# Performance work log

Measured on AMD Instinct MI355X. Metric: run time of the kernel, lower is better.

The kernel has to match this reference:

```python
import jax, jax.numpy as jnp
import numpy as np

NUM_EXPERTS = 8
HIDDEN = 2048
FFN = 1376
CAPACITY_FACTOR = 1.25
SCORE_SCALE = 1.0


def setup_inputs() -> dict:
    key = jax.random.key(0)
    k = jax.random.split(key, 6)
    T = 8192
    x = jax.random.normal(k[0], (T, HIDDEN), dtype=jnp.float32)
    topK_indices = jax.random.randint(k[1], (T,), 0, NUM_EXPERTS, dtype=jnp.int64)
    topK_scores = jax.random.uniform(k[2], (T,), dtype=jnp.float32)
    s = 1.0 / np.sqrt(HIDDEN)
    w_gate = jax.random.normal(k[3], (NUM_EXPERTS, HIDDEN, FFN), dtype=jnp.float32) * s
    w_up = jax.random.normal(k[4], (NUM_EXPERTS, HIDDEN, FFN), dtype=jnp.float32) * s
    w_down = jax.random.normal(k[5], (NUM_EXPERTS, FFN, HIDDEN), dtype=jnp.float32) * (1.0 / np.sqrt(FFN))
    return {"x": x, "topK_indices": topK_indices, "topK_scores": topK_scores,
            "w_gate": w_gate, "w_up": w_up, "w_down": w_down}


def reference(x, topK_indices, topK_scores, w_gate, w_up, w_down):
    T, D = x.shape
    E = w_gate.shape[0]
    capacity = int(CAPACITY_FACTOR * T / E)  # static (depends only on shapes)
    # position of each token within its assigned expert (deterministic drop:
    # keep the first `capacity` tokens in sequence order per expert)
    oh = jax.nn.one_hot(topK_indices, E, dtype=jnp.int32)          # [T,E]
    rank = jnp.take_along_axis(jnp.cumsum(oh, axis=0) - 1,
                               topK_indices[:, None].astype(jnp.int32), axis=1)[:, 0]
    keep = rank < capacity                                          # [T]
    # dispatch into per-expert capacity buffers; dropped tokens go to dummy slot
    slot = jnp.where(keep, topK_indices.astype(jnp.int32) * capacity + rank, E * capacity)
    buf = jnp.zeros((E * capacity + 1, D), x.dtype)
    buf = buf.at[slot].set(jnp.where(keep[:, None], x, jnp.zeros_like(x)))
    xe = buf[:E * capacity].reshape(E, capacity, D)                 # [E,C,D]
    # per-expert SwiGLU MLP as grouped GEMMs
    h = jax.nn.silu(jnp.einsum('ecd,edf->ecf', xe, w_gate)) * jnp.einsum('ecd,edf->ecf', xe, w_up)
    out = jnp.einsum('ecf,efd->ecd', h, w_down).reshape(E * capacity, D)
    out = jnp.concatenate([out, jnp.zeros((1, D), out.dtype)], axis=0)
    # combine: dropped tokens -> zero (dropped_padding='zero'), gate-score fusion
    y = out[slot] * keep[:, None].astype(out.dtype)
    y = y * (topK_scores[:, None] * SCORE_SCALE)
    return y
```

## Files before the change

kernel.cpp:

```cpp
#include <hip/hip_runtime.h>
#include <hip/hip_bf16.h>
#include <cstdint>
#include <cstddef>

#define NTOK 8192
#define DH   2048
#define DF   1376
#define DFP  1408
#define NE   8
#define CAP  1280

typedef __bf16 bf16x8 __attribute__((ext_vector_type(8)));
typedef float  f32x4  __attribute__((ext_vector_type(4)));

#define BARRIER() asm volatile("s_barrier" ::: "memory")
#define WAITV0()  asm volatile("s_waitcnt vmcnt(0)" ::: "memory")
#define WAITV4()  asm volatile("s_waitcnt vmcnt(4)" ::: "memory")
#define WAITV6()  asm volatile("s_waitcnt vmcnt(6)" ::: "memory")
#define SETPRIO(n) __builtin_amdgcn_s_setprio(n)

__device__ __forceinline__ uint32_t pk2(float a, float b) {
  float2 f; f.x = a; f.y = b;
  union { __hip_bfloat162 h; uint32_t u; } cv;
  cv.h = __float22bfloat162_rn(f);
  return cv.u;
}
__device__ __forceinline__ ushort bf16bits(float a) {
  return (ushort)(pk2(a, 0.f) & 0xFFFFu);
}
__device__ __forceinline__ void gload16(const ushort* g, ushort* l) {
  __builtin_amdgcn_global_load_lds(
      (const __attribute__((address_space(1))) uint32_t*)(const void*)g,
      (__attribute__((address_space(3))) uint32_t*)(void*)l,
      16, 0, 0);
}

__global__ void routing_kernel(const int* __restrict__ idx, int* __restrict__ tok_slot,
                               int* __restrict__ tok_keep) {
  __shared__ int cnt[256][NE];
  const int t = threadIdx.x;
  for (int s = t; s < NE * CAP; s += 256) tok_slot[s] = -1;
  unsigned long long cA = 0ull, cB = 0ull;
  const int per = NTOK / 256, base = t * per;
  for (int i = 0; i < per; ++i) {
    int e = idx[base + i];
    unsigned long long inc = 1ull << ((e & 3) * 16);
    if (e < 4) cA += inc; else cB += inc;
  }
#pragma unroll
  for (int e = 0; e < 4; ++e) cnt[t][e]     = (int)((cA >> (e * 16)) & 0xFFFF);
#pragma unroll
  for (int e = 0; e < 4; ++e) cnt[t][4 + e] = (int)((cB >> (e * 16)) & 0xFFFF);
  __syncthreads();
  if (t < NE) {
    int run = 0;
    for (int i = 0; i < 256; ++i) { int c = cnt[i][t]; cnt[i][t] = run; run += c; }
  }
  __syncthreads();
  cA = 0ull; cB = 0ull;
#pragma unroll
  for (int e = 0; e < 4; ++e) cA |= (unsigned long long)(cnt[t][e] & 0xFFFF) << (e * 16);
#pragma unroll
  for (int e = 0; e < 4; ++e) cB |= (unsigned long long)(cnt[t][4 + e] & 0xFFFF) << (e * 16);
  for (int i = 0; i < per; ++i) {
    int token = base + i;
    int e = idx[token];
    int sh = (e & 3) * 16;
    int r = (int)(((e < 4 ? cA : cB) >> sh) & 0xFFFF);
    unsigned long long inc = 1ull << sh;
    if (e < 4) cA += inc; else cB += inc;
    bool keep = (r < CAP);
    tok_keep[token] = keep ? 1 : 0;
    if (keep) tok_slot[e * CAP + r] = token;
  }
}

__global__ void zero_dropped(const int* __restrict__ keep, float* __restrict__ y) {
  if (keep[blockIdx.x]) return;
  float4 z = {0.f, 0.f, 0.f, 0.f};
  float* p = y + (size_t)blockIdx.x * DH + threadIdx.x * 8;
  *(float4*)p = z;
  *(float4*)(p + 4) = z;
}

__global__ void convert_x(const float* __restrict__ x, ushort* __restrict__ xb) {
  int i = (blockIdx.x * 256 + threadIdx.x) * 8;
  float4 a = *(const float4*)(x + i);
  float4 b = *(const float4*)(x + i + 4);
  uint4 p = { pk2(a.x, a.y), pk2(a.z, a.w), pk2(b.x, b.y), pk2(b.z, b.w) };
  *(uint4*)(xb + i) = p;
}

__global__ __launch_bounds__(256) void transpose_cvt(
    const float* __restrict__ in, ushort* __restrict__ out, int K, int N) {
  __shared__ ushort T[64][72];
  const int tid = threadIdx.x;
  const int n0 = blockIdx.x * 64, k0 = blockIdx.y * 64;
  const size_t eoff_in  = (size_t)blockIdx.z * K * N;
  const size_t eoff_out = (size_t)blockIdx.z * N * K;
  const int kr = tid >> 4;
  const int nc = (tid & 15) * 4;
#pragma unroll
  for (int it = 0; it < 4; ++it) {
    int k = k0 + kr + it * 16;
    int n = n0 + nc;
    float4 v = {0.f, 0.f, 0.f, 0.f};
    if (k < K && n + 4 <= N) v = *(const float4*)(in + eoff_in + (size_t)k * N + n);
    T[nc + 0][kr + it * 16] = bf16bits(v.x);
    T[nc + 1][kr + it * 16] = bf16bits(v.y);
    T[nc + 2][kr + it * 16] = bf16bits(v.z);
    T[nc + 3][kr + it * 16] = bf16bits(v.w);
  }
  __syncthreads();
  const int nr = tid >> 2;
  const int kc = tid & 3;
#pragma unroll
  for (int it = 0; it < 2; ++it) {
    int kloc = kc * 16 + it * 8;
    int n = n0 + nr, k = k0 + kloc;
    if (n < N && k + 8 <= K)
      *(uint4*)(out + eoff_out + (size_t)n * K + k) = *(const uint4*)&T[nr][kloc];
  }
}

__global__ void pad_h(ushort* __restrict__ h) {
  int idx = blockIdx.x * 512 + threadIdx.x;
  int row = idx >> 2, q = idx & 3;
  uint4 z = {0u, 0u, 0u, 0u};
  *(uint4*)(h + (size_t)row * DFP + DF + q * 8) = z;
}

__global__ __launch_bounds__(512, 1) void gemm_gateup3(
    const ushort* __restrict__ xb, const ushort* __restrict__ wgt,
    const ushort* __restrict__ wut, const int* __restrict__ tok_slot,
    ushort* __restrict__ h)
{
  __shared__ __align__(16) char smbuf[131072];
  char* sm = smbuf;
  const int tid = threadIdx.x, lane = tid & 63, wid = tid >> 6;
  const int wr = wid >> 1, wc = wid & 1;
  const int l15 = lane & 15, l4 = lane >> 4;

  int wgid = (blockIdx.x & 7) * 55 + (blockIdx.x >> 3);
  const int e = wgid / 55;
  const int rem = wgid - e * 55;
  const int mt = rem / 11, nt = rem - (rem / 11) * 11;
  const int n0 = nt * 128;

  const ushort* srcA[2][2]; const ushort* srcBg[2]; const ushort* srcBu[2];
#pragma unroll
  for (int u = 0; u < 2; ++u)
#pragma unroll
    for (int jj = 0; jj < 2; ++jj) {
      int o = u * 16384 + (jj * 8 + wid) * 1024 + lane * 16;
      int os = o ^ (((o >> 7) & 7) << 4);
      int row = os >> 7, kb = os & 127;
      int tk = tok_slot[e * CAP + mt * 256 + row];
      if (tk < 0) tk = 0;
      srcA[u][jj] = xb + (size_t)tk * DH + (kb >> 1);
    }
#pragma unroll
  for (int jj = 0; jj < 2; ++jj) {
    int o = (jj * 8 + wid) * 1024 + lane * 16;
    int os = o ^ (((o >> 7) & 7) << 4);
    int row = os >> 7, kb = os & 127;
    int n = n0 + row; if (n > DF - 1) n = DF - 1;
    srcBg[jj] = wgt + ((size_t)e * DF + n) * DH + (kb >> 1);
    srcBu[jj] = wut + ((size_t)e * DF + n) * DH + (kb >> 1);
  }
  int aoff0[4], aoff1[4], boff0[4], boff1[4];
#pragma unroll
  for (int i = 0; i < 4; ++i) {
    int row = wr * 64 + i * 16 + l15;
    int r4 = (row & 7) << 4;
    aoff0[i] = row * 128 + ((l4 * 16) ^ r4);
    aoff1[i] = row * 128 + ((l4 * 16 + 64) ^ r4);
  }
#pragma unroll
  for (int j = 0; j < 4; ++j) {
    int row = wc * 64 + j * 16 + l15;
    int r4 = (row & 7) << 4;
    boff0[j] = row * 128 + ((l4 * 16) ^ r4);
    boff1[j] = row * 128 + ((l4 * 16 + 64) ^ r4);
  }
  const int dst0 = wid * 1024, dst1 = (8 + wid) * 1024;

  f32x4 accG[4][4], accU[4][4];
#pragma unroll
  for (int i = 0; i < 4; ++i)
#pragma unroll
    for (int j = 0; j < 4; ++j) {
      accG[i][j] = (f32x4){0.f, 0.f, 0.f, 0.f};
      accU[i][j] = (f32x4){0.f, 0.f, 0.f, 0.f};
    }

  const int NT = DH / 64;
  gload16(srcA[0][0], (ushort*)(sm + dst0));
  gload16(srcA[0][1], (ushort*)(sm + dst1));
  gload16(srcA[1][0], (ushort*)(sm + 16384 + dst0));
  gload16(srcA[1][1], (ushort*)(sm + 16384 + dst1));
  gload16(srcBg[0],   (ushort*)(sm + 65536 + dst0));
  gload16(srcBg[1],   (ushort*)(sm + 65536 + dst1));
  gload16(srcBu[0],   (ushort*)(sm + 98304 + dst0));
  gload16(srcBu[1],   (ushort*)(sm + 98304 + dst1));
  gload16(srcA[0][0] + 64, (ushort*)(sm + 32768 + dst0));
  gload16(srcA[0][1] + 64, (ushort*)(sm + 32768 + dst1));
  gload16(srcA[1][0] + 64, (ushort*)(sm + 32768 + 16384 + dst0));
  gload16(srcA[1][1] + 64, (ushort*)(sm + 32768 + 16384 + dst1));
  gload16(srcBg[0] + 64,   (ushort*)(sm + 65536 + 16384 + dst0));
  gload16(srcBg[1] + 64,   (ushort*)(sm + 65536 + 16384 + dst1));
  WAITV6();
  BARRIER();

  bf16x8 a0[4], a1[4], bg[4], bu[4];
  for (int t = 0; t < NT; ++t) {
    const int p = t & 1;
    char* Ab  = sm + p * 32768;
    char* Bgb = sm + 65536 + p * 16384;
    char* Bub = sm + 98304 + p * 16384;
    char* Bun = sm + 98304 + (p ^ 1) * 16384;
#pragma unroll
    for (int i = 0; i < 4; ++i) a0[i] = *(const bf16x8*)(Ab + aoff0[i]);
#pragma unroll
    for (int j = 0; j < 4; ++j) bg[j] = *(const bf16x8*)(Bgb + boff0[j]);
    if (t + 1 < NT) {
      int kk = (t + 1) * 64;
      gload16(srcBu[0] + kk, (ushort*)(Bun + dst0));
      gload16(srcBu[1] + kk, (ushort*)(Bun + dst1));
    }
    BARRIER();
    SETPRIO(1);
#pragma unroll
    for (int j = 0; j < 4; ++j)
#pragma unroll
      for (int i = 0; i < 4; ++i)
        accG[i][j] = __builtin_amdgcn_mfma_f32_16x16x32_bf16(a0[i], bg[j], accG[i][j], 0, 0, 0);
    SETPRIO(0);
    BARRIER();
#pragma unroll
    for (int i = 0; i < 4; ++i) a1[i] = *(const bf16x8*)(Ab + aoff1[i]);
#pragma unroll
    for (int j = 0; j < 4; ++j) bg[j] = *(const bf16x8*)(Bgb + boff1[j]);
    BARRIER();
    SETPRIO(1);
#pragma unroll
    for (int j = 0; j < 4; ++j)
#pragma unroll
      for (int i = 0; i < 4; ++i)
        accG[i][j] = __builtin_amdgcn_mfma_f32_16x16x32_bf16(a1[i], bg[j], accG[i][j], 0, 0, 0);
    SETPRIO(0);
    BARRIER();
#pragma unroll
    for (int j = 0; j < 4; ++j) bu[j] = *(const bf16x8*)(Bub + boff0[j]);
    if (t + 2 < NT) {
      int kk = (t + 2) * 64;
      gload16(srcA[0][0] + kk, (ushort*)(Ab + dst0));
      gload16(srcA[0][1] + kk, (ushort*)(Ab + dst1));
      gload16(srcBg[0] + kk,   (ushort*)(Bgb + dst0));
      gload16(srcBg[1] + kk,   (ushort*)(Bgb + dst1));
    }
    BARRIER();
    SETPRIO(1);
#pragma unroll
    for (int j = 0; j < 4; ++j)
#pragma unroll
      for (int i = 0; i < 4; ++i)
        accU[i][j] = __builtin_amdgcn_mfma_f32_16x16x32_bf16(a0[i], bu[j], accU[i][j], 0, 0, 0);
    SETPRIO(0);
    BARRIER();
#pragma unroll
    for (int j = 0; j < 4; ++j) bu[j] = *(const bf16x8*)(Bub + boff1[j]);
    if (t + 2 < NT) {
      int kk = (t + 2) * 64;
      gload16(srcA[1][0] + kk, (ushort*)(Ab + 16384 + dst0));
      gload16(srcA[1][1] + kk, (ushort*)(Ab + 16384 + dst1));
    }
    BARRIER();
    SETPRIO(1);
#pragma unroll
    for (int j = 0; j < 4; ++j)
#pragma unroll
      for (int i = 0; i < 4; ++i)
        accU[i][j] = __builtin_amdgcn_mfma_f32_16x16x32_bf16(a1[i], bu[j], accU[i][j], 0, 0, 0);
    SETPRIO(0);
    if (t >= NT - 2) { WAITV0(); } else { WAITV6(); }
    BARRIER();
  }
  const size_t rowbase = (size_t)(e * CAP + mt * 256 + wr * 64);
#pragma unroll
  for (int j = 0; j < 4; ++j) {
    int col = n0 + wc * 64 + j * 16 + l15;
    if (col < DF) {
#pragma unroll
      for (int i = 0; i < 4; ++i)
#pragma unroll
        for (int r = 0; r < 4; ++r) {
          size_t row = rowbase + i * 16 + l4 * 4 + r;
          float gv = accG[i][j][r], uv = accU[i][j][r];
          h[row * DFP + col] = bf16bits(gv / (1.f + __expf(-gv)) * uv);
        }
    }
  }
}

__global__ __launch_bounds__(512, 1) void gemm_down3(
    const ushort* __restrict__ h, const ushort* __restrict__ wdt,
    const int* __restrict__ tok_slot, const float* __restrict__ scores,
    float* __restrict__ y)
{
  __shared__ __align__(16) char smbuf[100352];
  char* sm = smbuf;
  int* tokc = (int*)(sm + 98304);
  float* scc = (float*)(sm + 99328);
  const int tid = threadIdx.x, lane = tid & 63, wid = tid >> 6;
  const int wr = wid >> 1, wc = wid & 1;
  const int l15 = lane & 15, l4 = lane >> 4;

  int wgid = (blockIdx.x & 7) * 80 + (blockIdx.x >> 3);
  const int e = wgid / 80;
  const int rem = wgid - e * 80;
  const int mt = rem / 16, nt = rem & 15;
  const int n0 = nt * 128;

  if (tid < 256) {
    int tk = tok_slot[e * CAP + mt * 256 + tid];
    tokc[tid] = tk;
    scc[tid] = (tk >= 0) ? scores[tk] : 0.f;
  }
  __syncthreads();

  const size_t hrow0 = (size_t)(e * CAP + mt * 256);
  const ushort* srcA[2][2]; const ushort* srcB[2];
#pragma unroll
  for (int u = 0; u < 2; ++u)
#pragma unroll
    for (int jj = 0; jj < 2; ++jj) {
      int o = u * 16384 + (jj * 8 + wid) * 1024 + lane * 16;
      int os = o ^ (((o >> 7) & 7) << 4);
      int row = os >> 7, kb = os & 127;
      srcA[u][jj] = h + (hrow0 + row) * DFP + (kb >> 1);
    }
#pragma unroll
  for (int jj = 0; jj < 2; ++jj) {
    int o = (jj * 8 + wid) * 1024 + lane * 16;
    int os = o ^ (((o >> 7) & 7) << 4);
    int row = os >> 7, kb = os & 127;
    srcB[jj] = wdt + ((size_t)e * DH + n0 + row) * DF + (kb >> 1);
  }
  int aoff0[4], aoff1[4], boff0[4], boff1[4];
#pragma unroll
  for (int i = 0; i < 4; ++i) {
    int row = wr * 64 + i * 16 + l15;
    int r4 = (row & 7) << 4;
    aoff0[i] = row * 128 + ((l4 * 16) ^ r4);
    aoff1[i] = row * 128 + ((l4 * 16 + 64) ^ r4);
  }
#pragma unroll
  for (int j = 0; j < 4; ++j) {
    int row = wc * 64 + j * 16 + l15;
    int r4 = (row & 7) << 4;
    boff0[j] = row * 128 + ((l4 * 16) ^ r4);
    boff1[j] = row * 128 + ((l4 * 16 + 64) ^ r4);
  }
  const int dst0 = wid * 1024, dst1 = (8 + wid) * 1024;

  f32x4 acc[4][4];
#pragma unroll
  for (int i = 0; i < 4; ++i)
#pragma unroll
    for (int j = 0; j < 4; ++j) acc[i][j] = (f32x4){0.f, 0.f, 0.f, 0.f};

  const int NT = DFP / 64;
  gload16(srcA[0][0], (ushort*)(sm + dst0));
  gload16(srcA[0][1], (ushort*)(sm + dst1));
  gload16(srcA[1][0], (ushort*)(sm + 16384 + dst0));
  gload16(srcA[1][1], (ushort*)(sm + 16384 + dst1));
  gload16(srcB[0],    (ushort*)(sm + 65536 + dst0));
  gload16(srcB[1],    (ushort*)(sm + 65536 + dst1));
  gload16(srcA[0][0] + 64, (ushort*)(sm + 32768 + dst0));
  gload16(srcA[0][1] + 64, (ushort*)(sm + 32768 + dst1));
  gload16(srcA[1][0] + 64, (ushort*)(sm + 32768 + 16384 + dst0));
  gload16(srcA[1][1] + 64, (ushort*)(sm + 32768 + 16384 + dst1));
  WAITV4();
  BARRIER();

  bf16x8 a0[4], a1[4], b0, b1;
  for (int t = 0; t < NT; ++t) {
    const int p = t & 1;
    char* Ab = sm + p * 32768;
    char* Bb = sm + 65536 + p * 16384;
    char* Bn = sm + 65536 + (p ^ 1) * 16384;
#pragma unroll
    for (int i = 0; i < 4; ++i) a0[i] = *(const bf16x8*)(Ab + aoff0[i]);
    b0 = *(const bf16x8*)(Bb + boff0[0]);
    b1 = *(const bf16x8*)(Bb + boff0[1]);
    if (t + 1 < NT) {
      int kk = (t + 1) * 64;
      gload16(srcB[0] + kk, (ushort*)(Bn + dst0));
      gload16(srcB[1] + kk, (ushort*)(Bn + dst1));
    }
    BARRIER();
    SETPRIO(1);
#pragma unroll
    for (int i = 0; i < 4; ++i) {
      acc[i][0] = __builtin_amdgcn_mfma_f32_16x16x32_bf16(a0[i], b0, acc[i][0], 0, 0, 0);
      acc[i][1] = __builtin_amdgcn_mfma_f32_16x16x32_bf16(a0[i], b1, acc[i][1], 0, 0, 0);
    }
    SETPRIO(0);
    BARRIER();
    b0 = *(const bf16x8*)(Bb + boff0[2]);
    b1 = *(const bf16x8*)(Bb + boff0[3]);
    BARRIER();
    SETPRIO(1);
#pragma unroll
    for (int i = 0; i < 4; ++i) {
      acc[i][2] = __builtin_amdgcn_mfma_f32_16x16x32_bf16(a0[i], b0, acc[i][2], 0, 0, 0);
      acc[i][3] = __builtin_amdgcn_mfma_f32_16x16x32_bf16(a0[i], b1, acc[i][3], 0, 0, 0);
    }
    SETPRIO(0);
    BARRIER();
#pragma unroll
    for (int i = 0; i < 4; ++i) a1[i] = *(const bf16x8*)(Ab + aoff1[i]);
    b0 = *(const bf16x8*)(Bb + boff1[0]);
    b1 = *(const bf16x8*)(Bb + boff1[1]);
    BARRIER();
    SETPRIO(1);
#pragma unroll
    for (int i = 0; i < 4; ++i) {
      acc[i][0] = __builtin_amdgcn_mfma_f32_16x16x32_bf16(a1[i], b0, acc[i][0], 0, 0, 0);
      acc[i][1] = __builtin_amdgcn_mfma_f32_16x16x32_bf16(a1[i], b1, acc[i][1], 0, 0, 0);
    }
    SETPRIO(0);
    BARRIER();
    b0 = *(const bf16x8*)(Bb + boff1[2]);
    b1 = *(const bf16x8*)(Bb + boff1[3]);
    if (t + 2 < NT) {
      int kk = (t + 2) * 64;
      gload16(srcA[0][0] + kk, (ushort*)(Ab + dst0));
      gload16(srcA[0][1] + kk, (ushort*)(Ab + dst1));
      gload16(srcA[1][0] + kk, (ushort*)(Ab + 16384 + dst0));
      gload16(srcA[1][1] + kk, (ushort*)(Ab + 16384 + dst1));
    }
    BARRIER();
    SETPRIO(1);
#pragma unroll
    for (int i = 0; i < 4; ++i) {
      acc[i][2] = __builtin_amdgcn_mfma_f32_16x16x32_bf16(a1[i], b0, acc[i][2], 0, 0, 0);
      acc[i][3] = __builtin_amdgcn_mfma_f32_16x16x32_bf16(a1[i], b1, acc[i][3], 0, 0, 0);
    }
    SETPRIO(0);
    if (t >= NT - 2) { WAITV0(); } else { WAITV4(); }
    BARRIER();
  }
  int tkr[4][4]; float sr[4][4];
#pragma unroll
  for (int i = 0; i < 4; ++i)
#pragma unroll
    for (int r = 0; r < 4; ++r) {
      int rl = wr * 64 + i * 16 + l4 * 4 + r;
      tkr[i][r] = tokc[rl];
      sr[i][r]  = scc[rl];
    }
#pragma unroll
  for (int j = 0; j < 4; ++j) {
    int col = n0 + wc * 64 + j * 16 + l15;
#pragma unroll
    for (int i = 0; i < 4; ++i)
#pragma unroll
      for (int r = 0; r < 4; ++r)
        if (tkr[i][r] >= 0)
          y[(size_t)tkr[i][r] * DH + col] = acc[i][j][r] * sr[i][r];
  }
}

extern "C" void kernel_launch(void* const* d_in, const int* in_sizes, int n_in,
                              void* d_out, int out_size, void* d_ws, size_t ws_size,
                              hipStream_t stream) {
  const float* x   = (const float*)d_in[0];
  const int*   idx = (const int*)d_in[1];
  const float* sc  = (const float*)d_in[2];
  const float* wg  = (const float*)d_in[3];
  const float* wu  = (const float*)d_in[4];
  const float* wd  = (const float*)d_in[5];
  float* y = (float*)d_out;

  const size_t OFF_KEEP = 40960;
  const size_t OFF_H    = 73728;
  const size_t SZ_H     = (size_t)NE * CAP * DFP * 2;
  const size_t OFF_XB   = OFF_H + SZ_H;
  const size_t SZ_XB    = (size_t)NTOK * DH * 2;
  const size_t OFF_WGT  = OFF_XB + SZ_XB;
  const size_t SZ_W     = (size_t)NE * DH * DF * 2;
  const size_t OFF_WUT  = OFF_WGT + SZ_W;

  int* tok_slot = (int*)d_ws;
  int* tok_keep = (int*)((char*)d_ws + OFF_KEEP);
  ushort* hbuf = (ushort*)((char*)d_ws + OFF_H);
  ushort* xb   = (ushort*)((char*)d_ws + OFF_XB);
  ushort* wgt  = (ushort*)((char*)d_ws + OFF_WGT);
  ushort* wut  = (ushort*)((char*)d_ws + OFF_WUT);
  ushort* wdt  = wgt;

  hipLaunchKernelGGL(routing_kernel, dim3(1), dim3(256), 0, stream, idx, tok_slot, tok_keep);
  hipLaunchKernelGGL(zero_dropped, dim3(NTOK), dim3(256), 0, stream, tok_keep, y);
  hipLaunchKernelGGL(convert_x, dim3(NTOK * DH / 2048), dim3(256), 0, stream, x, xb);
  hipLaunchKernelGGL(transpose_cvt, dim3((DF + 63) / 64, DH / 64, NE), dim3(256), 0, stream,
                     wg, wgt, DH, DF);
  hipLaunchKernelGGL(transpose_cvt, dim3((DF + 63) / 64, DH / 64, NE), dim3(256), 0, stream,
                     wu, wut, DH, DF);
  hipLaunchKernelGGL(pad_h, dim3(80), dim3(512), 0, stream, hbuf);
  hipLaunchKernelGGL(gemm_gateup3, dim3(440), dim3(512), 0, stream,
                     xb, wgt, wut, tok_slot, hbuf);
  hipLaunchKernelGGL(transpose_cvt, dim3(DH / 64, (DF + 63) / 64, NE), dim3(256), 0, stream,
                     wd, wdt, DF, DH);
  hipLaunchKernelGGL(gemm_down3, dim3(640), dim3(512), 0, stream,
                     hbuf, wdt, tok_slot, sc, y);
}
```

Baseline: 333.9 us.

## Deepen LDS pipelines in both MoE GEMMs and drop intra-iteration barriers

```diff
diff --git a/kernel.cpp b/kernel.cpp
--- a/kernel.cpp
+++ b/kernel.cpp
@@ -15,8 +15,8 @@
 
 #define BARRIER() asm volatile("s_barrier" ::: "memory")
 #define WAITV0()  asm volatile("s_waitcnt vmcnt(0)" ::: "memory")
-#define WAITV4()  asm volatile("s_waitcnt vmcnt(4)" ::: "memory")
 #define WAITV6()  asm volatile("s_waitcnt vmcnt(6)" ::: "memory")
+#define WAITV8()  asm volatile("s_waitcnt vmcnt(8)" ::: "memory")
 #define SETPRIO(n) __builtin_amdgcn_s_setprio(n)
 
 __device__ __forceinline__ uint32_t pk2(float a, float b) {
@@ -135,8 +135,7 @@
     const ushort* __restrict__ wut, const int* __restrict__ tok_slot,
     ushort* __restrict__ h)
 {
-  __shared__ __align__(16) char smbuf[131072];
-  char* sm = smbuf;
+  __shared__ __align__(16) char sm[131072];
   const int tid = threadIdx.x, lane = tid & 63, wid = tid >> 6;
   const int wr = wid >> 1, wc = wid & 1;
   const int l15 = lane & 15, l4 = lane >> 4;
@@ -147,26 +146,149 @@
   const int mt = rem / 11, nt = rem - (rem / 11) * 11;
   const int n0 = nt * 128;
 
-  const ushort* srcA[2][2]; const ushort* srcBg[2]; const ushort* srcBu[2];
-#pragma unroll
-  for (int u = 0; u < 2; ++u)
-#pragma unroll
-    for (int jj = 0; jj < 2; ++jj) {
-      int o = u * 16384 + (jj * 8 + wid) * 1024 + lane * 16;
-      int os = o ^ (((o >> 7) & 7) << 4);
-      int row = os >> 7, kb = os & 127;
-      int tk = tok_slot[e * CAP + mt * 256 + row];
-      if (tk < 0) tk = 0;
-      srcA[u][jj] = xb + (size_t)tk * DH + (kb >> 1);
+  const ushort* srcA[2]; const ushort* srcBg; const ushort* srcBu;
+#pragma unroll
+  for (int c = 0; c < 2; ++c) {
+    int o = c * 8192 + wid * 1024 + lane * 16;
+    int os = o ^ (((o >> 6) & 3) << 4);
+    int row = os >> 6, kb = os & 63;
+    int tk = tok_slot[e * CAP + mt * 256 + row];
+    if (tk < 0) tk = 0;
+    srcA[c] = xb + (size_t)tk * DH + (kb >> 1);
+  }
+  {
+    int o = wid * 1024 + lane * 16;
+    int os = o ^ (((o >> 6) & 3) << 4);
+    int row = os >> 6, kb = os & 63;
+    int n = n0 + row; if (n > DF - 1) n = DF - 1;
+    srcBg = wgt + ((size_t)e * DF + n) * DH + (kb >> 1);
+    srcBu = wut + ((size_t)e * DF + n) * DH + (kb >> 1);
+  }
+  int aoff[4], boff[4];
+#pragma unroll
+  for (int i = 0; i < 4; ++i) {
+    int row = wr * 64 + i * 16 + l15;
+    aoff[i] = row * 64 + ((l4 * 16) ^ ((l15 & 3) << 4));
+  }
+#pragma unroll
+  for (int j = 0; j < 4; ++j) {
+    int row = wc * 64 + j * 16 + l15;
+    boff[j] = row * 64 + ((l4 * 16) ^ ((l15 & 3) << 4));
+  }
+  const int dstw = wid * 1024;
+
+  f32x4 accG[4][4], accU[4][4];
+#pragma unroll
+  for (int i = 0; i < 4; ++i)
+#pragma unroll
+    for (int j = 0; j < 4; ++j) {
+      accG[i][j] = (f32x4){0.f, 0.f, 0.f, 0.f};
+      accU[i][j] = (f32x4){0.f, 0.f, 0.f, 0.f};
     }
-#pragma unroll
-  for (int jj = 0; jj < 2; ++jj) {
-    int o = (jj * 8 + wid) * 1024 + lane * 16;
+
+  const int NT = DH / 32;
+#pragma unroll
+  for (int t0 = 0; t0 < 3; ++t0) {
+    int kk = t0 * 32;
+    gload16(srcA[0] + kk, (ushort*)(sm + t0 * 16384 + dstw));
+    gload16(srcA[1] + kk, (ushort*)(sm + t0 * 16384 + 8192 + dstw));
+    gload16(srcBg   + kk, (ushort*)(sm + 65536 + t0 * 8192 + dstw));
+    gload16(srcBu   + kk, (ushort*)(sm + 98304 + t0 * 8192 + dstw));
+  }
+  WAITV8();
+  BARRIER();
+
+  for (int t = 0; t < NT; ++t) {
+    const int r = t & 3, w = (t + 3) & 3;
+    char* Ab  = sm + r * 16384;
+    char* Bgb = sm + 65536 + r * 8192;
+    char* Bub = sm + 98304 + r * 8192;
+    bf16x8 a[4], bg[4], bu[4];
+#pragma unroll
+    for (int i = 0; i < 4; ++i) a[i]  = *(const bf16x8*)(Ab + aoff[i]);
+#pragma unroll
+    for (int j = 0; j < 4; ++j) bg[j] = *(const bf16x8*)(Bgb + boff[j]);
+#pragma unroll
+    for (int j = 0; j < 4; ++j) bu[j] = *(const bf16x8*)(Bub + boff[j]);
+    if (t + 3 < NT) {
+      int kk = (t + 3) * 32;
+      gload16(srcA[0] + kk, (ushort*)(sm + w * 16384 + dstw));
+      gload16(srcA[1] + kk, (ushort*)(sm + w * 16384 + 8192 + dstw));
+      gload16(srcBg   + kk, (ushort*)(sm + 65536 + w * 8192 + dstw));
+      gload16(srcBu   + kk, (ushort*)(sm + 98304 + w * 8192 + dstw));
+    }
+    SETPRIO(1);
+#pragma unroll
+    for (int j = 0; j < 4; ++j)
+#pragma unroll
+      for (int i = 0; i < 4; ++i)
+        accG[i][j] = __builtin_amdgcn_mfma_f32_16x16x32_bf16(a[i], bg[j], accG[i][j], 0, 0, 0);
+#pragma unroll
+    for (int j = 0; j < 4; ++j)
+#pragma unroll
+      for (int i = 0; i < 4; ++i)
+        accU[i][j] = __builtin_amdgcn_mfma_f32_16x16x32_bf16(a[i], bu[j], accU[i][j], 0, 0, 0);
+    SETPRIO(0);
+    if (t >= NT - 2) { WAITV0(); } else { WAITV8(); }
+    BARRIER();
+  }
+  const size_t rowbase = (size_t)(e * CAP + mt * 256 + wr * 64);
+#pragma unroll
+  for (int j = 0; j < 4; ++j) {
+    int col = n0 + wc * 64 + j * 16 + l15;
+    if (col < DF) {
+#pragma unroll
+      for (int i = 0; i < 4; ++i)
+#pragma unroll
+        for (int r2 = 0; r2 < 4; ++r2) {
+          size_t row = rowbase + i * 16 + l4 * 4 + r2;
+          float gv = accG[i][j][r2], uv = accU[i][j][r2];
+          h[row * DFP + col] = bf16bits(gv / (1.f + __expf(-gv)) * uv);
+        }
+    }
+  }
+}
+
+__global__ __launch_bounds__(512, 1) void gemm_down3(
+    const ushort* __restrict__ h, const ushort* __restrict__ wdt,
+    const int* __restrict__ tok_slot, const float* __restrict__ scores,
+    float* __restrict__ y)
+{
+  __shared__ __align__(16) char sm[149504];
+  int* tokc = (int*)(sm + 147456);
+  float* scc = (float*)(sm + 148480);
+  const int tid = threadIdx.x, lane = tid & 63, wid = tid >> 6;
+  const int wr = wid >> 1, wc = wid & 1;
+  const int l15 = lane & 15, l4 = lane >> 4;
+
+  int wgid = (blockIdx.x & 7) * 80 + (blockIdx.x >> 3);
+  const int e = wgid / 80;
+  const int rem = wgid - e * 80;
+  const int mt = rem / 16, nt = rem & 15;
+  const int n0 = nt * 128;
+
+  if (tid < 256) {
+    int tk = tok_slot[e * CAP + mt * 256 + tid];
+    tokc[tid] = tk;
+    scc[tid] = (tk >= 0) ? scores[tk] : 0.f;
+  }
+  __syncthreads();
+
+  const size_t hrow0 = (size_t)(e * CAP + mt * 256);
+  const ushort* srcA[4]; const ushort* srcB[2];
+#pragma unroll
+  for (int c = 0; c < 4; ++c) {
+    int o = c * 8192 + wid * 1024 + lane * 16;
     int os = o ^ (((o >> 7) & 7) << 4);
     int row = os >> 7, kb = os & 127;
-    int n = n0 + row; if (n > DF - 1) n = DF - 1;
-    srcBg[jj] = wgt + ((size_t)e * DF + n) * DH + (kb >> 1);
-    srcBu[jj] = wut + ((size_t)e * DF + n) * DH + (kb >> 1);
+    srcA[c] = h + (hrow0 + row) * DFP + (kb >> 1);
+  }
+#pragma unroll
+  for (int c = 0; c < 2; ++c) {
+    int o = c * 8192 + wid * 1024 + lane * 16;
+    int os = o ^ (((o >> 7) & 7) << 4);
+    int row = os >> 7, kb = os & 127;
+    srcB[c] = wdt + ((size_t)e * DH + n0 + row) * DF + (kb >> 1);
   }
   int aoff0[4], aoff1[4], boff0[4], boff1[4];
 #pragma unroll
@@ -183,274 +305,66 @@
     boff0[j] = row * 128 + ((l4 * 16) ^ r4);
     boff1[j] = row * 128 + ((l4 * 16 + 64) ^ r4);
   }
-  const int dst0 = wid * 1024, dst1 = (8 + wid) * 1024;
-
-  f32x4 accG[4][4], accU[4][4];
+  const int dstw = wid * 1024;
+
+  f32x4 acc[4][4];
 #pragma unroll
   for (int i = 0; i < 4; ++i)
 #pragma unroll
-    for (int j = 0; j < 4; ++j) {
-      accG[i][j] = (f32x4){0.f, 0.f, 0.f, 0.f};
-      accU[i][j] = (f32x4){0.f, 0.f, 0.f, 0.f};
-    }
-
-  const int NT = DH / 64;
-  gload16(srcA[0][0], (ushort*)(sm + dst0));
-  gload16(srcA[0][1], (ushort*)(sm + dst1));
-  gload16(srcA[1][0], (ushort*)(sm + 16384 + dst0));
-  gload16(srcA[1][1], (ushort*)(sm + 16384 + dst1));
-  gload16(srcBg[0],   (ushort*)(sm + 65536 + dst0));
-  gload16(srcBg[1],   (ushort*)(sm + 65536 + dst1));
-  gload16(srcBu[0],   (ushort*)(sm + 98304 + dst0));
-  gload16(srcBu[1],   (ushort*)(sm + 98304 + dst1));
-  gload16(srcA[0][0] + 64, (ushort*)(sm + 32768 + dst0));
-  gload16(srcA[0][1] + 64, (ushort*)(sm + 32768 + dst1));
-  gload16(srcA[1][0] + 64, (ushort*)(sm + 32768 + 16384 + dst0));
-  gload16(srcA[1][1] + 64, (ushort*)(sm + 32768 + 16384 + dst1));
-  gload16(srcBg[0] + 64,   (ushort*)(sm + 65536 + 16384 + dst0));
-  gload16(srcBg[1] + 64,   (ushort*)(sm + 65536 + 16384 + dst1));
+    for (int j = 0; j < 4; ++j) acc[i][j] = (f32x4){0.f, 0.f, 0.f, 0.f};
+
+  const int NT = DFP / 64;
+#pragma unroll
+  for (int t0 = 0; t0 < 2; ++t0) {
+    int kk = t0 * 64;
+#pragma unroll
+    for (int c = 0; c < 4; ++c)
+      gload16(srcA[c] + kk, (ushort*)(sm + t0 * 32768 + c * 8192 + dstw));
+#pragma unroll
+    for (int c = 0; c < 2; ++c)
+      gload16(srcB[c] + kk, (ushort*)(sm + 98304 + t0 * 16384 + c * 8192 + dstw));
+  }
   WAITV6();
   BARRIER();
 
-  bf16x8 a0[4], a1[4], bg[4], bu[4];
+  int rrot = 0, wrot = 2;
   for (int t = 0; t < NT; ++t) {
-    const int p = t & 1;
-    char* Ab  = sm + p * 32768;
-    char* Bgb = sm + 65536 + p * 16384;
-    char* Bub = sm + 98304 + p * 16384;
-    char* Bun = sm + 98304 + (p ^ 1) * 16384;
+    char* Ab = sm + rrot * 32768;
+    char* Bb = sm + 98304 + rrot * 16384;
+    bf16x8 a0[4], a1[4], b0[4], b1[4];
 #pragma unroll
     for (int i = 0; i < 4; ++i) a0[i] = *(const bf16x8*)(Ab + aoff0[i]);
 #pragma unroll
-    for (int j = 0; j < 4; ++j) bg[j] = *(const bf16x8*)(Bgb + boff0[j]);
-    if (t + 1 < NT) {
-      int kk = (t + 1) * 64;
-      gload16(srcBu[0] + kk, (ushort*)(Bun + dst0));
-      gload16(srcBu[1] + kk, (ushort*)(Bun + dst1));
-    }
-    BARRIER();
-    SETPRIO(1);
-#pragma unroll
-    for (int j = 0; j < 4; ++j)
-#pragma unroll
-      for (int i = 0; i < 4; ++i)
-        accG[i][j] = __builtin_amdgcn_mfma_f32_16x16x32_bf16(a0[i], bg[j], accG[i][j], 0, 0, 0);
-    SETPRIO(0);
-    BARRIER();
+    for (int j = 0; j < 4; ++j) b0[j] = *(const bf16x8*)(Bb + boff0[j]);
 #pragma unroll
     for (int i = 0; i < 4; ++i) a1[i] = *(const bf16x8*)(Ab + aoff1[i]);
 #pragma unroll
-    for (int j = 0; j < 4; ++j) bg[j] = *(const bf16x8*)(Bgb + boff1[j]);
-    BARRIER();
-    SETPRIO(1);
-#pragma unroll
-    for (int j = 0; j < 4; ++j)
-#pragma unroll
-      for (int i = 0; i < 4; ++i)
-        accG[i][j] = __builtin_amdgcn_mfma_f32_16x16x32_bf16(a1[i], bg[j], accG[i][j], 0, 0, 0);
-    SETPRIO(0);
-    BARRIER();
-#pragma unroll
-    for (int j = 0; j < 4; ++j) bu[j] = *(const bf16x8*)(Bub + boff0[j]);
+    for (int j = 0; j < 4; ++j) b1[j] = *(const bf16x8*)(Bb + boff1[j]);
     if (t + 2 < NT) {
       int kk = (t + 2) * 64;
-      gload16(srcA[0][0] + kk, (ushort*)(Ab + dst0));
-      gload16(srcA[0][1] + kk, (ushort*)(Ab + dst1));
-      gload16(srcBg[0] + kk,   (ushort*)(Bgb + dst0));
-      gload16(srcBg[1] + kk,   (ushort*)(Bgb + dst1));
+#pragma unroll
+      for (int c = 0; c < 4; ++c)
+        gload16(srcA[c] + kk, (ushort*)(sm + wrot * 32768 + c * 8192 + dstw));
+#pragma unroll
+      for (int c = 0; c < 2; ++c)
+        gload16(srcB[c] + kk, (ushort*)(sm + 98304 + wrot * 16384 + c * 8192 + dstw));
     }
-    BARRIER();
     SETPRIO(1);
 #pragma unroll
     for (int j = 0; j < 4; ++j)
 #pragma unroll
       for (int i = 0; i < 4; ++i)
-        accU[i][j] = __builtin_amdgcn_mfma_f32_16x16x32_bf16(a0[i], bu[j], accU[i][j], 0, 0, 0);
-    SETPRIO(0);
-    BARRIER();
-#pragma unroll
-    for (int j = 0; j < 4; ++j) bu[j] = *(const bf16x8*)(Bub + boff1[j]);
-    if (t + 2 < NT) {
-      int kk = (t + 2) * 64;
-      gload16(srcA[1][0] + kk, (ushort*)(Ab + 16384 + dst0));
-      gload16(srcA[1][1] + kk, (ushort*)(Ab + 16384 + dst1));
-    }
-    BARRIER();
-    SETPRIO(1);
+        acc[i][j] = __builtin_amdgcn_mfma_f32_16x16x32_bf16(a0[i], b0[j], acc[i][j], 0, 0, 0);
 #pragma unroll
     for (int j = 0; j < 4; ++j)
 #pragma unroll
       for (int i = 0; i < 4; ++i)
-        accU[i][j] = __builtin_amdgcn_mfma_f32_16x16x32_bf16(a1[i], bu[j], accU[i][j], 0, 0, 0);
+        acc[i][j] = __builtin_amdgcn_mfma_f32_16x16x32_bf16(a1[i], b1[j], acc[i][j], 0, 0, 0);
     SETPRIO(0);
     if (t >= NT - 2) { WAITV0(); } else { WAITV6(); }
     BARRIER();
-  }
-  const size_t rowbase = (size_t)(e * CAP + mt * 256 + wr * 64);
-#pragma unroll
-  for (int j = 0; j < 4; ++j) {
-    int col = n0 + wc * 64 + j * 16 + l15;
-    if (col < DF) {
-#pragma unroll
-      for (int i = 0; i < 4; ++i)
-#pragma unroll
-        for (int r = 0; r < 4; ++r) {
-          size_t row = rowbase + i * 16 + l4 * 4 + r;
-          float gv = accG[i][j][r], uv = accU[i][j][r];
-          h[row * DFP + col] = bf16bits(gv / (1.f + __expf(-gv)) * uv);
-        }
-    }
-  }
-}
-
-__global__ __launch_bounds__(512, 1) void gemm_down3(
-    const ushort* __restrict__ h, const ushort* __restrict__ wdt,
-    const int* __restrict__ tok_slot, const float* __restrict__ scores,
-    float* __restrict__ y)
-{
-  __shared__ __align__(16) char smbuf[100352];
-  char* sm = smbuf;
-  int* tokc = (int*)(sm + 98304);
-  float* scc = (float*)(sm + 99328);
-  const int tid = threadIdx.x, lane = tid & 63, wid = tid >> 6;
-  const int wr = wid >> 1, wc = wid & 1;
-  const int l15 = lane & 15, l4 = lane >> 4;
-
-  int wgid = (blockIdx.x & 7) * 80 + (blockIdx.x >> 3);
-  const int e = wgid / 80;
-  const int rem = wgid - e * 80;
-  const int mt = rem / 16, nt = rem & 15;
-  const int n0 = nt * 128;
-
-  if (tid < 256) {
-    int tk = tok_slot[e * CAP + mt * 256 + tid];
-    tokc[tid] = tk;
-    scc[tid] = (tk >= 0) ? scores[tk] : 0.f;
-  }
-  __syncthreads();
-
-  const size_t hrow0 = (size_t)(e * CAP + mt * 256);
-  const ushort* srcA[2][2]; const ushort* srcB[2];
-#pragma unroll
-  for (int u = 0; u < 2; ++u)
-#pragma unroll
-    for (int jj = 0; jj < 2; ++jj) {
-      int o = u * 16384 + (jj * 8 + wid) * 1024 + lane * 16;
-      int os = o ^ (((o >> 7) & 7) << 4);
-      int row = os >> 7, kb = os & 127;
-      srcA[u][jj] = h + (hrow0 + row) * DFP + (kb >> 1);
-    }
-#pragma unroll
-  for (int jj = 0; jj < 2; ++jj) {
-    int o = (jj * 8 + wid) * 1024 + lane * 16;
-    int os = o ^ (((o >> 7) & 7) << 4);
-    int row = os >> 7, kb = os & 127;
-    srcB[jj] = wdt + ((size_t)e * DH + n0 + row) * DF + (kb >> 1);
-  }
-  int aoff0[4], aoff1[4], boff0[4], boff1[4];
-#pragma unroll
-  for (int i = 0; i < 4; ++i) {
-    int row = wr * 64 + i * 16 + l15;
-    int r4 = (row & 7) << 4;
-    aoff0[i] = row * 128 + ((l4 * 16) ^ r4);
-    aoff1[i] = row * 128 + ((l4 * 16 + 64) ^ r4);
-  }
-#pragma unroll
-  for (int j = 0; j < 4; ++j) {
-    int row = wc * 64 + j * 16 + l15;
-    int r4 = (row & 7) << 4;
-    boff0[j] = row * 128 + ((l4 * 16) ^ r4);
-    boff1[j] = row * 128 + ((l4 * 16 + 64) ^ r4);
-  }
-  const int dst0 = wid * 1024, dst1 = (8 + wid) * 1024;
-
-  f32x4 acc[4][4];
-#pragma unroll
-  for (int i = 0; i < 4; ++i)
-#pragma unroll
-    for (int j = 0; j < 4; ++j) acc[i][j] = (f32x4){0.f, 0.f, 0.f, 0.f};
-
-  const int NT = DFP / 64;
-  gload16(srcA[0][0], (ushort*)(sm + dst0));
-  gload16(srcA[0][1], (ushort*)(sm + dst1));
-  gload16(srcA[1][0], (ushort*)(sm + 16384 + dst0));
-  gload16(srcA[1][1], (ushort*)(sm + 16384 + dst1));
-  gload16(srcB[0],    (ushort*)(sm + 65536 + dst0));
-  gload16(srcB[1],    (ushort*)(sm + 65536 + dst1));
-  gload16(srcA[0][0] + 64, (ushort*)(sm + 32768 + dst0));
-  gload16(srcA[0][1] + 64, (ushort*)(sm + 32768 + dst1));
-  gload16(srcA[1][0] + 64, (ushort*)(sm + 32768 + 16384 + dst0));
-  gload16(srcA[1][1] + 64, (ushort*)(sm + 32768 + 16384 + dst1));
-  WAITV4();
-  BARRIER();
-
-  bf16x8 a0[4], a1[4], b0, b1;
-  for (int t = 0; t < NT; ++t) {
-    const int p = t & 1;
-    char* Ab = sm + p * 32768;
-    char* Bb = sm + 65536 + p * 16384;
-    char* Bn = sm + 65536 + (p ^ 1) * 16384;
-#pragma unroll
-    for (int i = 0; i < 4; ++i) a0[i] = *(const bf16x8*)(Ab + aoff0[i]);
-    b0 = *(const bf16x8*)(Bb + boff0[0]);
-    b1 = *(const bf16x8*)(Bb + boff0[1]);
-    if (t + 1 < NT) {
-      int kk = (t + 1) * 64;
-      gload16(srcB[0] + kk, (ushort*)(Bn + dst0));
-      gload16(srcB[1] + kk, (ushort*)(Bn + dst1));
-    }
-    BARRIER();
-    SETPRIO(1);
-#pragma unroll
-    for (int i = 0; i < 4; ++i) {
-      acc[i][0] = __builtin_amdgcn_mfma_f32_16x16x32_bf16(a0[i], b0, acc[i][0], 0, 0, 0);
-      acc[i][1] = __builtin_amdgcn_mfma_f32_16x16x32_bf16(a0[i], b1, acc[i][1], 0, 0, 0);
-    }
-    SETPRIO(0);
-    BARRIER();
-    b0 = *(const bf16x8*)(Bb + boff0[2]);
-    b1 = *(const bf16x8*)(Bb + boff0[3]);
-    BARRIER();
-    SETPRIO(1);
-#pragma unroll
-    for (int i = 0; i < 4; ++i) {
-      acc[i][2] = __builtin_amdgcn_mfma_f32_16x16x32_bf16(a0[i], b0, acc[i][2], 0, 0, 0);
-      acc[i][3] = __builtin_amdgcn_mfma_f32_16x16x32_bf16(a0[i], b1, acc[i][3], 0, 0, 0);
-    }
-    SETPRIO(0);
-    BARRIER();
-#pragma unroll
-    for (int i = 0; i < 4; ++i) a1[i] = *(const bf16x8*)(Ab + aoff1[i]);
-    b0 = *(const bf16x8*)(Bb + boff1[0]);
-    b1 = *(const bf16x8*)(Bb + boff1[1]);
-    BARRIER();
-    SETPRIO(1);
-#pragma unroll
-    for (int i = 0; i < 4; ++i) {
-      acc[i][0] = __builtin_amdgcn_mfma_f32_16x16x32_bf16(a1[i], b0, acc[i][0], 0, 0, 0);
-      acc[i][1] = __builtin_amdgcn_mfma_f32_16x16x32_bf16(a1[i], b1, acc[i][1], 0, 0, 0);
-    }
-    SETPRIO(0);
-    BARRIER();
-    b0 = *(const bf16x8*)(Bb + boff1[2]);
-    b1 = *(const bf16x8*)(Bb + boff1[3]);
-    if (t + 2 < NT) {
-      int kk = (t + 2) * 64;
-      gload16(srcA[0][0] + kk, (ushort*)(Ab + dst0));
-      gload16(srcA[0][1] + kk, (ushort*)(Ab + dst1));
-      gload16(srcA[1][0] + kk, (ushort*)(Ab + 16384 + dst0));
-      gload16(srcA[1][1] + kk, (ushort*)(Ab + 16384 + dst1));
-    }
-    BARRIER();
-    SETPRIO(1);
-#pragma unroll
-    for (int i = 0; i < 4; ++i) {
-      acc[i][2] = __builtin_amdgcn_mfma_f32_16x16x32_bf16(a1[i], b0, acc[i][2], 0, 0, 0);
-      acc[i][3] = __builtin_amdgcn_mfma_f32_16x16x32_bf16(a1[i], b1, acc[i][3], 0, 0, 0);
-    }
-    SETPRIO(0);
-    if (t >= NT - 2) { WAITV0(); } else { WAITV4(); }
-    BARRIER();
+    rrot = (rrot == 2) ? 0 : rrot + 1;
+    wrot = (wrot == 2) ? 0 : wrot + 1;
   }
   int tkr[4][4]; float sr[4][4];
 #pragma unroll
```

Result: slower. 350.0 us (+4.8%).
